# Performance work log

Measured on AMD Instinct MI355X. Metric: run time of the kernel, lower is better.

The kernel has to match this reference:

```python
import math
import jax, jax.numpy as jnp
import numpy as np

B, T, E, H = 1, 2048, 2048, 16
D = E // H // 2  # head_dim = 64
DEPTH = 12
LAMBDA_INIT = 0.8 - 0.6 * math.exp(-0.3 * DEPTH)
EPS = 1e-5
NEG = -1e30


def rotary_cos_sin(seqlen, dim):
    # matches flash-attn RotaryEmbedding: inv_freq over even indices, base 10000
    inv_freq = 1.0 / (10000.0 ** (jnp.arange(0, dim, 2, dtype=jnp.float32) / dim))
    t = jnp.arange(seqlen, dtype=jnp.float32)
    freqs = jnp.outer(t, inv_freq)  # [T, D/2]
    return jnp.cos(freqs), jnp.sin(freqs)


def apply_rotary_interleaved(x, cos, sin):
    # x: [B, T, nH, D]; rotate interleaved pairs (x0,x1),(x2,x3),...
    x1 = x[..., 0::2]
    x2 = x[..., 1::2]
    c = cos[None, :, None, :]
    s = sin[None, :, None, :]
    o1 = x1 * c - x2 * s
    o2 = x1 * s + x2 * c
    return jnp.stack([o1, o2], axis=-1).reshape(x.shape)


def causal_attn_pair(q, k, v1, v2, mask, scale):
    # q,k,v*: [B, T, H, D]; shared softmax over (q,k), applied to both v1 and v2
    s = jnp.einsum('bthd,bshd->bhts', q, k) * scale
    s = jnp.where(mask, s, NEG)
    a = jax.nn.softmax(s, axis=-1)
    o1 = jnp.einsum('bhts,bshd->bthd', a, v1)
    o2 = jnp.einsum('bhts,bshd->bthd', a, v2)
    return jnp.concatenate([o1, o2], axis=-1)  # [B, T, H, 2D]


def setup_inputs() -> dict:
    key = jax.random.key(0)
    ks = jax.random.split(key, 10)
    return {
        'query': jax.random.normal(ks[0], (B, T, E), dtype=jnp.float32),
        'Wq': jax.random.normal(ks[1], (E, E), dtype=jnp.float32) * 0.02,
        'Wk': jax.random.normal(ks[2], (E, E), dtype=jnp.float32) * 0.02,
        'Wv': jax.random.normal(ks[3], (E, E), dtype=jnp.float32) * 0.02,
        'Wout': jax.random.normal(ks[4], (E, E), dtype=jnp.float32) * 0.02,
        'lambda_q1': jax.random.normal(ks[5], (D,), dtype=jnp.float32) * 0.1,
        'lambda_k1': jax.random.normal(ks[6], (D,), dtype=jnp.float32) * 0.1,
        'lambda_q2': jax.random.normal(ks[7], (D,), dtype=jnp.float32) * 0.1,
        'lambda_k2': jax.random.normal(ks[8], (D,), dtype=jnp.float32) * 0.1,
        'rms_weight': jnp.ones((2 * D,), dtype=jnp.float32),
    }


def reference(query, Wq, Wk, Wv, Wout, lambda_q1, lambda_k1, lambda_q2, lambda_k2, rms_weight):
    bsz, tgt_len, embed_dim = query.shape
    cos, sin = rotary_cos_sin(tgt_len, D)
    scale = D ** (-0.5)
    mask = jnp.tril(jnp.ones((tgt_len, tgt_len), dtype=bool))[None, None]

    q = (query @ Wq).reshape(bsz, tgt_len, 2 * H, D)
    k = (query @ Wk).reshape(bsz, tgt_len, 2 * H, D)
    v = (query @ Wv).reshape(bsz, tgt_len, H, 2, D)

    q = apply_rotary_emb = apply_rotary_interleaved(q, cos, sin)
    k = apply_rotary_interleaved(k, cos, sin)

    q = q.reshape(bsz, tgt_len, H, 2, D)
    k = k.reshape(bsz, tgt_len, H, 2, D)
    q1, q2 = q[:, :, :, 0], q[:, :, :, 1]
    k1, k2 = k[:, :, :, 0], k[:, :, :, 1]
    v1, v2 = v[:, :, :, 0], v[:, :, :, 1]

    attn1 = causal_attn_pair(q1, k1, v1, v2, mask, scale)  # [B,T,H,2D]
    attn2 = causal_attn_pair(q2, k2, v1, v2, mask, scale)

    lambda_1 = jnp.exp(jnp.sum(lambda_q1 * lambda_k1))
    lambda_2 = jnp.exp(jnp.sum(lambda_q2 * lambda_k2))
    lambda_full = lambda_1 - lambda_2 + LAMBDA_INIT

    f1 = jnp.fft.rfft(attn1, axis=1)
    f2 = jnp.fft.rfft(attn2, axis=1)
    attn_freq = f1 - lambda_full * f2

    n_freq = attn_freq.shape[1]
    sigma = 0.3 / 2.0  # cutoff_ratio / 2, gaussian window
    x = jnp.linspace(0.0, 1.0, n_freq)
    filt = jnp.exp(-0.5 * (x / sigma) ** 2)
    attn_freq = attn_freq * filt[None, :, None, None]

    attn = jnp.fft.irfft(attn_freq, n=tgt_len, axis=1)  # [B,T,H,2D]

    # RMSNorm over last dim (2*head_dim) with affine weight
    attn = attn * jax.lax.rsqrt(jnp.mean(attn * attn, axis=-1, keepdims=True) + EPS) * rms_weight
    attn = attn * (1.0 - LAMBDA_INIT)

    attn = attn.reshape(bsz, tgt_len, H * 2 * D)
    return attn @ Wout
```

## Files before the change

kernel.cpp:

```cpp
#include <hip/hip_runtime.h>
#include <math.h>

#define LAMBDA_INIT_F 0.7836057665316245f
#define ONE_MINUS_LI  0.2163942334683755f

typedef unsigned short ushort_t;
typedef unsigned int   uint32;
typedef unsigned long long u64;
typedef __attribute__((ext_vector_type(8))) short short8;
typedef __attribute__((ext_vector_type(4))) float f32x4;

__device__ __forceinline__ ushort_t f2bf(float f) {
    union { float f; uint32 u; } x; x.f = f;
    uint32 r = (x.u + 0x7fffu + ((x.u >> 16) & 1u)) >> 16;
    return (ushort_t)r;
}

__device__ __forceinline__ void gld16(ushort_t* lds, const ushort_t* g) {
    __builtin_amdgcn_global_load_lds(
        (const __attribute__((address_space(1))) uint32*)g,
        (__attribute__((address_space(3))) uint32*)lds,
        16, 0, 0);
}

__global__ __launch_bounds__(64) void lambda_kernel(
    const float* __restrict__ lq1, const float* __restrict__ lk1,
    const float* __restrict__ lq2, const float* __restrict__ lk2,
    float* __restrict__ lam)
{
    int l = threadIdx.x;
    float p1 = lq1[l] * lk1[l];
    float p2 = lq2[l] * lk2[l];
    for (int off = 32; off; off >>= 1) {
        p1 += __shfl_down(p1, off);
        p2 += __shfl_down(p2, off);
    }
    if (l == 0) lam[0] = expf(p1) - expf(p2) + LAMBDA_INIT_F;
}

__global__ __launch_bounds__(256) void gfilt_kernel(float* __restrict__ g)
{
    __shared__ float red[4];
    const int j = blockIdx.x;
    int tau = j - 64;
    int ta = tau < 0 ? -tau : tau;
    const int tid = threadIdx.x;
    float acc = 0.0f;
    for (int k = tid; k <= 1024; k += 256) {
        float w = (k == 0 || k == 1024) ? 1.0f : 2.0f;
        float r = (float)k * (1.0f / 153.6f);
        float f = expf(-0.5f * r * r);
        int m = (k * ta) & 2047;
        float ang = (float)m * 3.0679615757712823e-3f;
        acc += w * f * cosf(ang);
    }
    for (int off = 32; off; off >>= 1) acc += __shfl_down(acc, off);
    if ((tid & 63) == 0) red[tid >> 6] = acc;
    __syncthreads();
    if (tid == 0)
        g[j] = (red[0] + red[1] + red[2] + red[3]) * (1.0f / 2048.0f);
}

__global__ __launch_bounds__(256) void rottab(float* __restrict__ ct, float* __restrict__ st)
{
    int id = blockIdx.x * 256 + threadIdx.x;
    int t = id >> 5, i = id & 31;
    double inv = exp(-0.28782313662425575 * (double)i);
    double a = (double)t * inv;
    ct[id] = (float)cos(a);
    st[id] = (float)sin(a);
}

__global__ __launch_bounds__(256) void cvt_bf16(const float* __restrict__ s, ushort_t* __restrict__ d)
{
    int i = (blockIdx.x * 256 + threadIdx.x) * 8;
    float4 a = *(const float4*)(s + i);
    float4 b = *(const float4*)(s + i + 4);
    uint4 pk;
    pk.x = (uint32)f2bf(a.x) | ((uint32)f2bf(a.y) << 16);
    pk.y = (uint32)f2bf(a.z) | ((uint32)f2bf(a.w) << 16);
    pk.z = (uint32)f2bf(b.x) | ((uint32)f2bf(b.y) << 16);
    pk.w = (uint32)f2bf(b.z) | ((uint32)f2bf(b.w) << 16);
    *(uint4*)(d + i) = pk;
}

__global__ __launch_bounds__(256) void wtrans(
    const float* __restrict__ Wq, const float* __restrict__ Wk,
    const float* __restrict__ Wv, const float* __restrict__ Wo,
    ushort_t* __restrict__ Tq, ushort_t* __restrict__ Tk,
    ushort_t* __restrict__ Tv, ushort_t* __restrict__ To)
{
    int z = blockIdx.z;
    const float* S = (z == 0) ? Wq : (z == 1) ? Wk : (z == 2) ? Wv : Wo;
    ushort_t* Dt = (z == 0) ? Tq : (z == 1) ? Tk : (z == 2) ? Tv : To;
    bool perm = (z < 2);
    __shared__ float Ls[64 * 65];
    const int tid = threadIdx.x;
    const int n0 = blockIdx.x * 64, k0 = blockIdx.y * 64;
    #pragma unroll
    for (int it = 0; it < 4; ++it) {
        int kk = it * 16 + (tid >> 4);
        int nn = (tid & 15) * 4;
        float4 v = *(const float4*)(S + (size_t)(k0 + kk) * 2048 + n0 + nn);
        Ls[(nn + 0) * 65 + kk] = v.x;
        Ls[(nn + 1) * 65 + kk] = v.y;
        Ls[(nn + 2) * 65 + kk] = v.z;
        Ls[(nn + 3) * 65 + kk] = v.w;
    }
    __syncthreads();
    int nl = tid >> 2, kc = (tid & 3) * 16;
    int ng = n0 + nl;
    int nd = perm ? ((ng & ~63) | ((ng & 1) << 5) | ((ng & 63) >> 1)) : ng;
    uint4 p0, p1;
    const float* row = Ls + nl * 65 + kc;
    p0.x = (uint32)f2bf(row[0])  | ((uint32)f2bf(row[1])  << 16);
    p0.y = (uint32)f2bf(row[2])  | ((uint32)f2bf(row[3])  << 16);
    p0.z = (uint32)f2bf(row[4])  | ((uint32)f2bf(row[5])  << 16);
    p0.w = (uint32)f2bf(row[6])  | ((uint32)f2bf(row[7])  << 16);
    p1.x = (uint32)f2bf(row[8])  | ((uint32)f2bf(row[9])  << 16);
    p1.y = (uint32)f2bf(row[10]) | ((uint32)f2bf(row[11]) << 16);
    p1.z = (uint32)f2bf(row[12]) | ((uint32)f2bf(row[13]) << 16);
    p1.w = (uint32)f2bf(row[14]) | ((uint32)f2bf(row[15]) << 16);
    *(uint4*)(Dt + (size_t)nd * 2048 + k0 + kc) = p0;
    *(uint4*)(Dt + (size_t)nd * 2048 + k0 + kc + 8) = p1;
}

__global__ __launch_bounds__(256) void gemm_qkv(
    const ushort_t* __restrict__ A, const ushort_t* __restrict__ WT,
    ushort_t* __restrict__ q1, ushort_t* __restrict__ q2,
    ushort_t* __restrict__ k1, ushort_t* __restrict__ k2,
    ushort_t* __restrict__ v1T, ushort_t* __restrict__ v2T,
    const float* __restrict__ ctab, const float* __restrict__ stab)
{
    __shared__ ushort_t As[8192];
    __shared__ ushort_t Bs[8192];
    const int tid = threadIdx.x;
    const int w = tid >> 6, lane = tid & 63;
    const int quad = lane >> 4, l15 = lane & 15;
    const int wr = w >> 1, wc = w & 1;
    const int rb = blockIdx.y * 128, cb = blockIdx.x * 128;

    f32x4 acc[4][4];
    #pragma unroll
    for (int i = 0; i < 4; ++i)
        #pragma unroll
        for (int j = 0; j < 4; ++j) acc[i][j] = (f32x4)0.0f;

    for (int k0 = 0; k0 < 2048; k0 += 64) {
        #pragma unroll
        for (int u = 0; u < 4; ++u) {
            int off = (w * 4 + u) * 512;
            int Lc = (off >> 3) + lane;
            int row = Lc >> 3, cc = (Lc & 7) ^ (row & 7);
            gld16(As + off, A + (size_t)(rb + row) * 2048 + k0 + cc * 8);
            gld16(Bs + off, WT + (size_t)(cb + row) * 2048 + k0 + cc * 8);
        }
        __syncthreads();
        #pragma unroll
        for (int ks = 0; ks < 2; ++ks) {
            short8 af[4], bfr[4];
            #pragma unroll
            for (int mi = 0; mi < 4; ++mi) {
                int r = wr * 64 + mi * 16 + l15;
                af[mi] = *(const short8*)(As + r * 64 + ((ks * 4 + quad) ^ (r & 7)) * 8);
            }
            #pragma unroll
            for (int nj = 0; nj < 4; ++nj) {
                int r = wc * 64 + nj * 16 + l15;
                bfr[nj] = *(const short8*)(Bs + r * 64 + ((ks * 4 + quad) ^ (r & 7)) * 8);
            }
            #pragma unroll
            for (int mi = 0; mi < 4; ++mi)
                #pragma unroll
                for (int nj = 0; nj < 4; ++nj)
                    acc[mi][nj] = __builtin_amdgcn_mfma_f32_16x16x32_bf16(
                        af[mi], bfr[nj], acc[mi][nj], 0, 0, 0);
        }
        __syncthreads();
    }

    const int region = cb >> 11;
    const int nloc = cb & 2047;
    if (region < 2) {
        int head2 = (nloc + wc * 64) >> 6;
        ushort_t* b1 = region ? k1 : q1;
        ushort_t* b2 = region ? k2 : q2;
        ushort_t* dst = ((head2 & 1) ? b2 : b1) + (size_t)(head2 >> 1) * 2048 * 64;
        #pragma unroll
        for (int mi = 0; mi < 4; ++mi)
            #pragma unroll
            for (int r = 0; r < 4; ++r) {
                int t = rb + wr * 64 + mi * 16 + quad * 4 + r;
                const float* ctr = ctab + t * 32;
                const float* str = stab + t * 32;
                #pragma unroll
                for (int nj = 0; nj < 2; ++nj) {
                    int i = nj * 16 + l15;
                    float c = ctr[i], s = str[i];
                    float x1 = acc[mi][nj][r], x2 = acc[mi][nj + 2][r];
                    dst[(size_t)t * 64 + i]      = f2bf(x1 * c - x2 * s);
                    dst[(size_t)t * 64 + 32 + i] = f2bf(x1 * s + x2 * c);
                }
            }
    } else {
        #pragma unroll
        for (int mi = 0; mi < 4; ++mi)
            #pragma unroll
            for (int nj = 0; nj < 4; ++nj) {
                int cg = nloc + wc * 64 + nj * 16 + l15;
                int hh = cg >> 7, pr = (cg >> 6) & 1, d = cg & 63;
                int tb = rb + wr * 64 + mi * 16 + quad * 4;
                ushort_t* dst = (pr ? v2T : v1T) + ((size_t)(hh * 64 + d)) * 2048 + tb;
                u64 pk = (u64)f2bf(acc[mi][nj][0])
                       | ((u64)f2bf(acc[mi][nj][1]) << 16)
                       | ((u64)f2bf(acc[mi][nj][2]) << 32)
                       | ((u64)f2bf(acc[mi][nj][3]) << 48);
                *(u64*)dst = pk;
            }
    }
}

#define PSTRIDE 88

__device__ __forceinline__ void attn_step(
    const ushort_t* __restrict__ Kb, const ushort_t* __restrict__ V1b,
    const ushort_t* __restrict__ V2b, ushort_t* __restrict__ pw,
    const short8* qb, f32x4* O, float& m_i, float& l_i,
    int quad, int l15, int row_l, bool diag)
{
    f32x4 s[4];
    #pragma unroll
    for (int j = 0; j < 4; ++j) s[j] = (f32x4)0.0f;
    #pragma unroll
    for (int ks = 0; ks < 2; ++ks)
        #pragma unroll
        for (int j = 0; j < 4; ++j) {
            int r = j * 16 + l15;
            short8 kf = *(const short8*)(Kb + r * 64 + ((ks * 4 + quad) ^ (r & 7)) * 8);
            s[j] = __builtin_amdgcn_mfma_f32_16x16x32_bf16(kf, qb[ks], s[j], 0, 0, 0);
        }
    float mx = -1e30f;
    #pragma unroll
    for (int j = 0; j < 4; ++j)
        #pragma unroll
        for (int r = 0; r < 4; ++r) {
            float v = s[j][r] * 0.125f;
            if (diag) {
                int kp = j * 16 + quad * 4 + r;
                v = (kp <= row_l) ? v : -1e30f;
            }
            s[j][r] = v;
            mx = fmaxf(mx, v);
        }
    mx = fmaxf(mx, __shfl_xor(mx, 16));
    mx = fmaxf(mx, __shfl_xor(mx, 32));
    float newm = fmaxf(m_i, mx);
    float alpha = __expf(m_i - newm);
    float sum = 0.0f;
    #pragma unroll
    for (int j = 0; j < 4; ++j) {
        float p0 = __expf(s[j][0] - newm);
        float p1 = __expf(s[j][1] - newm);
        float p2 = __expf(s[j][2] - newm);
        float p3 = __expf(s[j][3] - newm);
        sum += (p0 + p1) + (p2 + p3);
        u64 pk = (u64)f2bf(p0) | ((u64)f2bf(p1) << 16)
               | ((u64)f2bf(p2) << 32) | ((u64)f2bf(p3) << 48);
        *(u64*)(pw + l15 * PSTRIDE + j * 16 + quad * 4) = pk;
    }
    sum += __shfl_xor(sum, 16);
    sum += __shfl_xor(sum, 32);
    l_i = l_i * alpha + sum;
    m_i = newm;
    float av0 = __shfl(alpha, quad * 4 + 0);
    float av1 = __shfl(alpha, quad * 4 + 1);
    float av2 = __shfl(alpha, quad * 4 + 2);
    float av3 = __shfl(alpha, quad * 4 + 3);
    #pragma unroll
    for (int nt = 0; nt < 8; ++nt) {
        O[nt][0] *= av0; O[nt][1] *= av1; O[nt][2] *= av2; O[nt][3] *= av3;
    }
    #pragma unroll
    for (int ks = 0; ks < 2; ++ks) {
        short8 pf = *(const short8*)(pw + l15 * PSTRIDE + ks * 32 + quad * 8);
        #pragma unroll
        for (int nt = 0; nt < 8; ++nt) {
            const ushort_t* Vs = (nt < 4) ? V1b : V2b;
            int d = (nt & 3) * 16 + l15;
            short8 vf = *(const short8*)(Vs + d * 64 + ((ks * 4 + quad) ^ (d & 7)) * 8);
            O[nt] = __builtin_amdgcn_mfma_f32_16x16x32_bf16(pf, vf, O[nt], 0, 0, 0);
        }
    }
}

__global__ __launch_bounds__(512, 4) void attn_pipe(
    const ushort_t* __restrict__ q1, const ushort_t* __restrict__ k1,
    const ushort_t* __restrict__ q2, const ushort_t* __restrict__ k2,
    const ushort_t* __restrict__ v1T, const ushort_t* __restrict__ v2T,
    float* __restrict__ X, const float* __restrict__ lam_ptr)
{
    __shared__ ushort_t Tt[4][4096];
    __shared__ ushort_t Ps[8][16 * PSTRIDE];

    const int tid = threadIdx.x;
    const int w = tid >> 6, lane = tid & 63;
    const int quad = lane >> 4, l15 = lane & 15;
    const int pair = w >> 2, wl = w & 3;
    const int b = blockIdx.x;
    const int h = b & 15;
    const int x16 = (b & 255) >> 4;
    const int qt = (b < 256) ? (31 - x16) : x16;
    const float lam = lam_ptr[0];
    const int row_l = wl * 16 + l15;

    const ushort_t* k1h = k1 + (size_t)h * 2048 * 64;
    const ushort_t* k2h = k2 + (size_t)h * 2048 * 64;
    const ushort_t* v1h = v1T + (size_t)h * 64 * 2048;
    const ushort_t* v2h = v2T + (size_t)h * 64 * 2048;

    short8 qb[2];
    {
        const ushort_t* qp = (pair ? q2 : q1)
            + ((size_t)h * 2048 + qt * 64 + wl * 16 + l15) * 64 + quad * 8;
        qb[0] = *(const short8*)(qp);
        qb[1] = *(const short8*)(qp + 32);
    }

    const int ci = tid;
    const int srow = ci >> 3, scc = (ci & 7) ^ (srow & 7);
    const int koff = srow * 64 + scc * 8;
    const int voff = srow * 2048 + scc * 8;

    short8 sK1, sK2, sV1, sV2;

    sK1 = *(const short8*)(k1h + koff);
    sK2 = *(const short8*)(k2h + koff);
    sV1 = *(const short8*)(v1h + voff);
    sV2 = *(const short8*)(v2h + voff);
    *(short8*)(&Tt[0][ci * 8]) = sK1;
    *(short8*)(&Tt[1][ci * 8]) = sK2;
    *(short8*)(&Tt[2][ci * 8]) = sV1;
    *(short8*)(&Tt[3][ci * 8]) = sV2;
    __syncthreads();

    f32x4 O[8];
    #pragma unroll
    for (int i = 0; i < 8; ++i) O[i] = (f32x4)0.0f;
    float m_i = -1e30f, l_i = 0.0f;

    const ushort_t* Kb = Tt[pair];

    for (int kt = 0; kt <= qt; ++kt) {
        if (kt < qt) {
            int kb = (kt + 1) * 4096, vb = (kt + 1) * 64;
            sK1 = *(const short8*)(k1h + kb + koff);
            sK2 = *(const short8*)(k2h + kb + koff);
            sV1 = *(const short8*)(v1h + vb + voff);
            sV2 = *(const short8*)(v2h + vb + voff);
        }
        attn_step(Kb, Tt[2], Tt[3], &Ps[w][0], qb, O, m_i, l_i,
                  quad, l15, row_l, kt == qt);
        __syncthreads();
        if (kt < qt) {
            *(short8*)(&Tt[0][ci * 8]) = sK1;
            *(short8*)(&Tt[1][ci * 8]) = sK2;
            *(short8*)(&Tt[2][ci * 8]) = sV1;
            *(short8*)(&Tt[3][ci * 8]) = sV2;
            __syncthreads();
        }
    }

    float sc = pair ? lam : 1.0f;
    float rr0 = sc / __shfl(l_i, quad * 4 + 0);
    float rr1 = sc / __shfl(l_i, quad * 4 + 1);
    float rr2 = sc / __shfl(l_i, quad * 4 + 2);
    float rr3 = sc / __shfl(l_i, quad * 4 + 3);

    float* LX = (float*)&Tt[0][0];
    const int rbase = wl * 16 + quad * 4;
    if (pair) {
        #pragma unroll
        for (int nt = 0; nt < 8; ++nt) {
            int cb = nt * 16 + l15;
            LX[(rbase + 0) * 128 + cb] = O[nt][0] * rr0;
            LX[(rbase + 1) * 128 + cb] = O[nt][1] * rr1;
            LX[(rbase + 2) * 128 + cb] = O[nt][2] * rr2;
            LX[(rbase + 3) * 128 + cb] = O[nt][3] * rr3;
        }
    }
    __syncthreads();
    if (!pair) {
        int tb = qt * 64 + rbase;
        #pragma unroll
        for (int nt = 0; nt < 8; ++nt) {
            int cb = nt * 16 + l15;
            int col = h * 128 + cb;
            X[(size_t)(tb + 0) * 2048 + col] = O[nt][0] * rr0 - LX[(rbase + 0) * 128 + cb];
            X[(size_t)(tb + 1) * 2048 + col] = O[nt][1] * rr1 - LX[(rbase + 1) * 128 + cb];
            X[(size_t)(tb + 2) * 2048 + col] = O[nt][2] * rr2 - LX[(rbase + 2) * 128 + cb];
            X[(size_t)(tb + 3) * 2048 + col] = O[nt][3] * rr3 - LX[(rbase + 3) * 128 + cb];
        }
    }
}

__global__ __launch_bounds__(256) void conv_t(
    const float* __restrict__ X, const float* __restrict__ g, float* __restrict__ Y)
{
    __shared__ float Xs[192 * 64];
    __shared__ float gs[129];
    const int tid = threadIdx.x;
    const int c0 = blockIdx.x * 64, t0 = blockIdx.y * 64;
    const int c = tid & 63, tg = tid >> 6;
    for (int j = tg; j < 192; j += 4)
        Xs[j * 64 + c] = X[(size_t)((t0 - 64 + j) & 2047) * 2048 + c0 + c];
    if (tid < 129) gs[tid] = g[tid];
    __syncthreads();
    float accv[16];
    #pragma unroll
    for (int i = 0; i < 16; ++i) accv[i] = 0.0f;
    const int tl0 = tg * 16;
    for (int tap = 0; tap < 129; ++tap) {
        float gv = gs[tap];
        int base = (tl0 + 128 - tap) * 64 + c;
        #pragma unroll
        for (int i = 0; i < 16; ++i) accv[i] += gv * Xs[base + i * 64];
    }
    #pragma unroll
    for (int i = 0; i < 16; ++i)
        Y[(size_t)(t0 + tl0 + i) * 2048 + c0 + c] = accv[i];
}

__global__ __launch_bounds__(64) void rms_bf(
    const float* __restrict__ Y, const float* __restrict__ wgt, ushort_t* __restrict__ yb)
{
    int grp = blockIdx.x;
    int t = grp >> 4, hh = grp & 15, l = threadIdx.x;
    size_t base = (size_t)t * 2048 + hh * 128;
    float a = Y[base + l];
    float b = Y[base + 64 + l];
    float ss = a * a + b * b;
    for (int off = 32; off; off >>= 1) ss += __shfl_down(ss, off);
    ss = __shfl(ss, 0);
    float r = rsqrtf(ss * (1.0f / 128.0f) + 1e-5f) * ONE_MINUS_LI;
    yb[base + l]      = f2bf(a * r * wgt[l]);
    yb[base + 64 + l] = f2bf(b * r * wgt[64 + l]);
}

__global__ __launch_bounds__(256) void gemm_out(
    const ushort_t* __restrict__ A, const ushort_t* __restrict__ BT,
    float* __restrict__ C)
{
    __shared__ ushort_t As[4096];
    __shared__ ushort_t Bs[8192];
    const int tid = threadIdx.x;
    const int w = tid >> 6, lane = tid & 63;
    const int quad = lane >> 4, l15 = lane & 15;
    const int wr = w >> 1, wc = w & 1;
    const int rb = blockIdx.y * 64, cb = blockIdx.x * 128;

    f32x4 acc[2][4];
    #pragma unroll
    for (int i = 0; i < 2; ++i)
        #pragma unroll
        for (int j = 0; j < 4; ++j) acc[i][j] = (f32x4)0.0f;

    for (int k0 = 0; k0 < 2048; k0 += 64) {
        #pragma unroll
        for (int u = 0; u < 2; ++u) {
            int off = (w * 2 + u) * 512;
            int Lc = (off >> 3) + lane;
            int row = Lc >> 3, cc = (Lc & 7) ^ (row & 7);
            gld16(As + off, A + (size_t)(rb + row) * 2048 + k0 + cc * 8);
        }
        #pragma unroll
        for (int u = 0; u < 4; ++u) {
            int off = (w * 4 + u) * 512;
            int Lc = (off >> 3) + lane;
            int row = Lc >> 3, cc = (Lc & 7) ^ (row & 7);
            gld16(Bs + off, BT + (size_t)(cb + row) * 2048 + k0 + cc * 8);
        }
        __syncthreads();
        #pragma unroll
        for (int ks = 0; ks < 2; ++ks) {
            short8 af[2], bfr[4];
            #pragma unroll
            for (int mi = 0; mi < 2; ++mi) {
                int r = wr * 32 + mi * 16 + l15;
                af[mi] = *(const short8*)(As + r * 64 + ((ks * 4 + quad) ^ (r & 7)) * 8);
            }
            #pragma unroll
            for (int nj = 0; nj < 4; ++nj) {
                int r = wc * 64 + nj * 16 + l15;
                bfr[nj] = *(const short8*)(Bs + r * 64 + ((ks * 4 + quad) ^ (r & 7)) * 8);
            }
            #pragma unroll
            for (int mi = 0; mi < 2; ++mi)
                #pragma unroll
                for (int nj = 0; nj < 4; ++nj)
                    acc[mi][nj] = __builtin_amdgcn_mfma_f32_16x16x32_bf16(
                        af[mi], bfr[nj], acc[mi][nj], 0, 0, 0);
        }
        __syncthreads();
    }

    #pragma unroll
    for (int mi = 0; mi < 2; ++mi)
        #pragma unroll
        for (int nj = 0; nj < 4; ++nj) {
            int cg = cb + wc * 64 + nj * 16 + l15;
            #pragma unroll
            for (int r = 0; r < 4; ++r) {
                int t = rb + wr * 32 + mi * 16 + quad * 4 + r;
                C[(size_t)t * 2048 + cg] = acc[mi][nj][r];
            }
        }
}

extern "C" void kernel_launch(void* const* d_in, const int* in_sizes, int n_in,
                              void* d_out, int out_size, void* d_ws, size_t ws_size,
                              hipStream_t stream)
{
    const float* query = (const float*)d_in[0];
    const float* Wq    = (const float*)d_in[1];
    const float* Wk    = (const float*)d_in[2];
    const float* Wv    = (const float*)d_in[3];
    const float* Wout  = (const float*)d_in[4];
    const float* lq1   = (const float*)d_in[5];
    const float* lk1   = (const float*)d_in[6];
    const float* lq2   = (const float*)d_in[7];
    const float* lk2   = (const float*)d_in[8];
    const float* rmsw  = (const float*)d_in[9];
    float* out = (float*)d_out;

    const size_t MB = 1ull << 20;
    char* W = (char*)d_ws;
    ushort_t* WqT   = (ushort_t*)(W + 0 * MB);
    ushort_t* WkT   = (ushort_t*)(W + 8 * MB);
    ushort_t* WvT   = (ushort_t*)(W + 16 * MB);
    ushort_t* WoutT = (ushort_t*)(W + 24 * MB);
    ushort_t* qb    = (ushort_t*)(W + 32 * MB);
    ushort_t* q1    = (ushort_t*)(W + 40 * MB);
    ushort_t* q2    = (ushort_t*)(W + 44 * MB);
    ushort_t* k1    = (ushort_t*)(W + 48 * MB);
    ushort_t* k2    = (ushort_t*)(W + 52 * MB);
    ushort_t* v1T   = (ushort_t*)(W + 56 * MB);
    ushort_t* v2T   = (ushort_t*)(W + 60 * MB);
    float*    X     = (float*)   (W + 64 * MB);
    float*    Y     = (float*)   (W + 32 * MB);
    ushort_t* ybf   = (ushort_t*)(W + 48 * MB);
    float*    ctab  = (float*)   (W + 80 * MB);
    float*    stab  = (float*)   (W + 80 * MB + 256 * 1024);
    float*    gbuf  = (float*)   (W + 80 * MB + 512 * 1024);
    float*    lam   = (float*)   (W + 80 * MB + 520 * 1024);

    lambda_kernel<<<1, 64, 0, stream>>>(lq1, lk1, lq2, lk2, lam);
    gfilt_kernel<<<129, 256, 0, stream>>>(gbuf);
    rottab<<<256, 256, 0, stream>>>(ctab, stab);
    cvt_bf16<<<2048, 256, 0, stream>>>(query, qb);
    wtrans<<<dim3(32, 32, 4), 256, 0, stream>>>(Wq, Wk, Wv, Wout, WqT, WkT, WvT, WoutT);

    gemm_qkv<<<dim3(48, 16), 256, 0, stream>>>(qb, WqT, q1, q2, k1, k2, v1T, v2T, ctab, stab);

    attn_pipe<<<512, 512, 0, stream>>>(q1, k1, q2, k2, v1T, v2T, X, lam);

    conv_t<<<dim3(32, 32), 256, 0, stream>>>(X, gbuf, Y);
    rms_bf<<<32768, 64, 0, stream>>>(Y, rmsw, ybf);

    gemm_out<<<dim3(16, 32), 256, 0, stream>>>(ybf, WoutT, out);
}
```

Baseline: 344.0 us.

## Restructure QKV GEMM into 256x256 tiles with double-buffered quadrant pipelining

```diff
diff --git a/kernel.cpp b/kernel.cpp
--- a/kernel.cpp
+++ b/kernel.cpp
@@ -125,91 +125,153 @@
     *(uint4*)(Dt + (size_t)nd * 2048 + k0 + kc + 8) = p1;
 }
 
-__global__ __launch_bounds__(256) void gemm_qkv(
+template<int QA, int QB, bool RA>
+__device__ __forceinline__ void qkv_phase(
+    const ushort_t* __restrict__ Ah, const ushort_t* __restrict__ Bh,
+    short8 af[8], f32x4 acc[8][4], int wr, int wc, int quad, int l15)
+{
+    if (RA) {
+        #pragma unroll
+        for (int m = 0; m < 4; ++m)
+            #pragma unroll
+            for (int ks = 0; ks < 2; ++ks) {
+                int r = wr * 64 + m * 16 + l15;
+                af[m * 2 + ks] = *(const short8*)(Ah + r * 64 + ((ks * 4 + quad) ^ (r & 7)) * 8);
+            }
+    }
+    short8 bfr[4];
+    #pragma unroll
+    for (int n = 0; n < 2; ++n)
+        #pragma unroll
+        for (int ks = 0; ks < 2; ++ks) {
+            int r = (wc >> 1) * 64 + (wc & 1) * 16 + n * 32 + l15;
+            bfr[n * 2 + ks] = *(const short8*)(Bh + r * 64 + ((ks * 4 + quad) ^ (r & 7)) * 8);
+        }
+    __builtin_amdgcn_s_setprio(1);
+    #pragma unroll
+    for (int m = 0; m < 4; ++m)
+        #pragma unroll
+        for (int n = 0; n < 2; ++n)
+            #pragma unroll
+            for (int ks = 0; ks < 2; ++ks)
+                acc[QA * 4 + m][QB * 2 + n] = __builtin_amdgcn_mfma_f32_16x16x32_bf16(
+                    af[m * 2 + ks], bfr[n * 2 + ks], acc[QA * 4 + m][QB * 2 + n], 0, 0, 0);
+    __builtin_amdgcn_s_setprio(0);
+}
+
+#define PH_SYNC() do { __builtin_amdgcn_s_barrier(); __builtin_amdgcn_sched_barrier(0); } while (0)
+
+__global__ __launch_bounds__(512, 2) void gemm_qkv(
     const ushort_t* __restrict__ A, const ushort_t* __restrict__ WT,
     ushort_t* __restrict__ q1, ushort_t* __restrict__ q2,
     ushort_t* __restrict__ k1, ushort_t* __restrict__ k2,
     ushort_t* __restrict__ v1T, ushort_t* __restrict__ v2T,
     const float* __restrict__ ctab, const float* __restrict__ stab)
 {
-    __shared__ ushort_t As[8192];
-    __shared__ ushort_t Bs[8192];
+    __shared__ ushort_t As[2][2][8192];
+    __shared__ ushort_t Bs[2][2][8192];
     const int tid = threadIdx.x;
     const int w = tid >> 6, lane = tid & 63;
     const int quad = lane >> 4, l15 = lane & 15;
-    const int wr = w >> 1, wc = w & 1;
-    const int rb = blockIdx.y * 128, cb = blockIdx.x * 128;
-
-    f32x4 acc[4][4];
-    #pragma unroll
-    for (int i = 0; i < 4; ++i)
+    const int wr = w >> 2, wc = w & 3;
+    const int rb = blockIdx.y * 256, cbg = blockIdx.x * 256;
+
+    auto stageA = [&](int pr, int ha, int tau) {
+        int k0 = tau * 64;
+        #pragma unroll
+        for (int u = 0; u < 2; ++u) {
+            int ci = w * 128 + u * 64 + lane;
+            int row = ci >> 3, cc = (ci & 7) ^ (row & 7);
+            gld16(&As[pr][ha][(w * 128 + u * 64) * 8],
+                  A + (size_t)(rb + ha * 128 + row) * 2048 + k0 + cc * 8);
+        }
+    };
+    auto stageB = [&](int pr, int hb, int tau) {
+        int k0 = tau * 64;
+        #pragma unroll
+        for (int u = 0; u < 2; ++u) {
+            int ci = w * 128 + u * 64 + lane;
+            int row = ci >> 3, cc = (ci & 7) ^ (row & 7);
+            gld16(&Bs[pr][hb][(w * 128 + u * 64) * 8],
+                  WT + (size_t)(cbg + hb * 128 + row) * 2048 + k0 + cc * 8);
+        }
+    };
+
+    stageA(0, 0, 0); stageB(0, 0, 0);
+    stageA(0, 1, 0); stageB(0, 1, 0);
+    stageA(1, 0, 1); stageB(1, 0, 1);
+
+    f32x4 acc[8][4];
+    #pragma unroll
+    for (int i = 0; i < 8; ++i)
         #pragma unroll
         for (int j = 0; j < 4; ++j) acc[i][j] = (f32x4)0.0f;
-
-    for (int k0 = 0; k0 < 2048; k0 += 64) {
-        #pragma unroll
-        for (int u = 0; u < 4; ++u) {
-            int off = (w * 4 + u) * 512;
-            int Lc = (off >> 3) + lane;
-            int row = Lc >> 3, cc = (Lc & 7) ^ (row & 7);
-            gld16(As + off, A + (size_t)(rb + row) * 2048 + k0 + cc * 8);
-            gld16(Bs + off, WT + (size_t)(cb + row) * 2048 + k0 + cc * 8);
-        }
-        __syncthreads();
-        #pragma unroll
-        for (int ks = 0; ks < 2; ++ks) {
-            short8 af[4], bfr[4];
-            #pragma unroll
-            for (int mi = 0; mi < 4; ++mi) {
-                int r = wr * 64 + mi * 16 + l15;
-                af[mi] = *(const short8*)(As + r * 64 + ((ks * 4 + quad) ^ (r & 7)) * 8);
-            }
-            #pragma unroll
-            for (int nj = 0; nj < 4; ++nj) {
-                int r = wc * 64 + nj * 16 + l15;
-                bfr[nj] = *(const short8*)(Bs + r * 64 + ((ks * 4 + quad) ^ (r & 7)) * 8);
-            }
-            #pragma unroll
-            for (int mi = 0; mi < 4; ++mi)
-                #pragma unroll
-                for (int nj = 0; nj < 4; ++nj)
-                    acc[mi][nj] = __builtin_amdgcn_mfma_f32_16x16x32_bf16(
-                        af[mi], bfr[nj], acc[mi][nj], 0, 0, 0);
-        }
-        __syncthreads();
-    }
-
-    const int region = cb >> 11;
-    const int nloc = cb & 2047;
+    short8 af[8];
+
+    for (int it = 0; it < 16; ++it) {
+        const int t = it * 2;
+        const int t2 = (t + 2 < 32) ? t + 2 : 31;
+        const int t3 = (t + 3 < 32) ? t + 3 : 31;
+        asm volatile("s_waitcnt vmcnt(8)" ::: "memory");
+        PH_SYNC();
+        stageA(1, 1, t + 1);
+        qkv_phase<0, 0, true >(As[0][0], Bs[0][0], af, acc, wr, wc, quad, l15);
+        asm volatile("s_waitcnt vmcnt(6)" ::: "memory");
+        PH_SYNC();
+        stageB(1, 1, t + 1);
+        qkv_phase<0, 1, false>(As[0][0], Bs[0][1], af, acc, wr, wc, quad, l15);
+        PH_SYNC();
+        stageA(0, 0, t2);
+        qkv_phase<1, 0, true >(As[0][1], Bs[0][0], af, acc, wr, wc, quad, l15);
+        PH_SYNC();
+        stageB(0, 0, t2);
+        qkv_phase<1, 1, false>(As[0][1], Bs[0][1], af, acc, wr, wc, quad, l15);
+        asm volatile("s_waitcnt vmcnt(8)" ::: "memory");
+        PH_SYNC();
+        stageA(0, 1, t2);
+        qkv_phase<0, 0, true >(As[1][0], Bs[1][0], af, acc, wr, wc, quad, l15);
+        asm volatile("s_waitcnt vmcnt(6)" ::: "memory");
+        PH_SYNC();
+        stageB(0, 1, t2);
+        qkv_phase<0, 1, false>(As[1][0], Bs[1][1], af, acc, wr, wc, quad, l15);
+        PH_SYNC();
+        stageA(1, 0, t3);
+        qkv_phase<1, 0, true >(As[1][1], Bs[1][0], af, acc, wr, wc, quad, l15);
+        PH_SYNC();
+        stageB(1, 0, t3);
+        qkv_phase<1, 1, false>(As[1][1], Bs[1][1], af, acc, wr, wc, quad, l15);
+    }
+
+    const int region = cbg >> 11;
+    const int nloc = cbg & 2047;
     if (region < 2) {
-        int head2 = (nloc + wc * 64) >> 6;
         ushort_t* b1 = region ? k1 : q1;
         ushort_t* b2 = region ? k2 : q2;
-        ushort_t* dst = ((head2 & 1) ? b2 : b1) + (size_t)(head2 >> 1) * 2048 * 64;
-        #pragma unroll
-        for (int mi = 0; mi < 4; ++mi)
-            #pragma unroll
-            for (int r = 0; r < 4; ++r) {
-                int t = rb + wr * 64 + mi * 16 + quad * 4 + r;
-                const float* ctr = ctab + t * 32;
-                const float* str = stab + t * 32;
+        const int i = (wc & 1) * 16 + l15;
+        #pragma unroll
+        for (int qb = 0; qb < 2; ++qb) {
+            int head2 = (nloc >> 6) + qb * 2 + (wc >> 1);
+            ushort_t* dst = ((head2 & 1) ? b2 : b1) + (size_t)(head2 >> 1) * 2048 * 64;
+            #pragma unroll
+            for (int mi = 0; mi < 8; ++mi)
                 #pragma unroll
-                for (int nj = 0; nj < 2; ++nj) {
-                    int i = nj * 16 + l15;
-                    float c = ctr[i], s = str[i];
-                    float x1 = acc[mi][nj][r], x2 = acc[mi][nj + 2][r];
+                for (int r = 0; r < 4; ++r) {
+                    int t = rb + (mi >> 2) * 128 + wr * 64 + (mi & 3) * 16 + quad * 4 + r;
+                    float c = ctab[t * 32 + i], s = stab[t * 32 + i];
+                    float x1 = acc[mi][qb * 2 + 0][r], x2 = acc[mi][qb * 2 + 1][r];
                     dst[(size_t)t * 64 + i]      = f2bf(x1 * c - x2 * s);
                     dst[(size_t)t * 64 + 32 + i] = f2bf(x1 * s + x2 * c);
                 }
-            }
+        }
     } else {
         #pragma unroll
-        for (int mi = 0; mi < 4; ++mi)
+        for (int mi = 0; mi < 8; ++mi)
             #pragma unroll
             for (int nj = 0; nj < 4; ++nj) {
-                int cg = nloc + wc * 64 + nj * 16 + l15;
+                int cg = nloc + (nj >> 1) * 128 + (wc >> 1) * 64 + (wc & 1) * 16
+                       + (nj & 1) * 32 + l15;
                 int hh = cg >> 7, pr = (cg >> 6) & 1, d = cg & 63;
-                int tb = rb + wr * 64 + mi * 16 + quad * 4;
+                int tb = rb + (mi >> 2) * 128 + wr * 64 + (mi & 3) * 16 + quad * 4;
                 ushort_t* dst = (pr ? v2T : v1T) + ((size_t)(hh * 64 + d)) * 2048 + tb;
                 u64 pk = (u64)f2bf(acc[mi][nj][0])
                        | ((u64)f2bf(acc[mi][nj][1]) << 16)
@@ -559,7 +621,7 @@
     cvt_bf16<<<2048, 256, 0, stream>>>(query, qb);
     wtrans<<<dim3(32, 32, 4), 256, 0, stream>>>(Wq, Wk, Wv, Wout, WqT, WkT, WvT, WoutT);
 
-    gemm_qkv<<<dim3(48, 16), 256, 0, stream>>>(qb, WqT, q1, q2, k1, k2, v1T, v2T, ctab, stab);
+    gemm_qkv<<<dim3(24, 8), 512, 0, stream>>>(qb, WqT, q1, q2, k1, k2, v1T, v2T, ctab, stab);
 
     attn_pipe<<<512, 512, 0, stream>>>(q1, k1, q2, k2, v1T, v2T, X, lam);
 
```

Result: no change. 337.8 us (-1.8%).
